# Optimization experiments

Hardware: AMD Instinct MI355X
Metric: run time of the kernel (lower is better)

The kernel has to match this reference:

```python
import jax, jax.numpy as jnp
import numpy as np
import math

M = 0.5
S = 64.0
TH = math.cos(math.pi - M)           # threshold cos(pi - m)
MM = math.sin(math.pi - M) * M       # sin(pi - m) * m
EPS = 1e-12

def _l2norm(x, axis=-1):
    return x / jnp.sqrt(jnp.sum(x * x, axis=axis, keepdims=True) + EPS)

def setup_inputs() -> dict:
    key = jax.random.key(0)
    k1, k2, k3 = jax.random.split(key, 3)
    B, D, C = 512, 512, 100000
    features = jax.random.normal(k1, (B, D), dtype=jnp.float32)
    weight = jax.random.normal(k2, (C, D), dtype=jnp.float32)
    labels = jax.random.randint(k3, (B,), 0, C, dtype=jnp.int32)
    return {"features": features, "labels": labels, "weight": weight}

def reference(features, labels, weight):
    # cos_theta: [B, C] = normalized features @ normalized weight^T
    cos_theta = jnp.einsum('bd,cd->bc', _l2norm(features), _l2norm(weight))
    cos_theta = jnp.clip(cos_theta, -1.0, 1.0)
    B = features.shape[0]
    rows = jnp.arange(B)
    # margin correction only affects the target column per row; gather it
    tgt_cos = cos_theta[rows, labels]                      # [B]
    theta_m = jnp.arccos(tgt_cos) + M
    cos_theta_m = jnp.cos(theta_m)
    tgt_adj = jnp.where(tgt_cos > TH, cos_theta_m, tgt_cos - MM)
    output = cos_theta.at[rows, labels].set(tgt_adj)
    return S * output
```

## Files before the change

### kernel.cpp

```cpp
#include <hip/hip_runtime.h>
#include <hip/hip_bf16.h>


typedef __attribute__((ext_vector_type(8))) short short8;
typedef __attribute__((ext_vector_type(8))) unsigned short u16x8;
typedef __attribute__((ext_vector_type(4))) float f32x4;

#define TH_CONST  (-0.8775825618903728f)
#define MM_CONST  (0.23971276930210156f)
#define M_MARGIN  0.5f
#define S_SCALE   64.0f

#define BM 128
#define BN 128
#define BK 32
#define KD 512

__device__ __forceinline__ unsigned short f2bf(float x) {
    unsigned int u = __float_as_uint(x);
    u += 0x7fffu + ((u >> 16) & 1u);
    return (unsigned short)(u >> 16);
}

__global__ __launch_bounds__(256, 2)
void arcface_kernel(const float* __restrict__ F,
                    const int*   __restrict__ labels,
                    const float* __restrict__ W,
                    float*       __restrict__ Out,
                    const int C)
{
    __shared__ unsigned short As[BM][BK];
    __shared__ unsigned short Bs[BN][BK];
    __shared__ float normF[BM];
    __shared__ float normW[BN];
    __shared__ int   Ls[BM];

    const int t = threadIdx.x;
    const int m_base = blockIdx.x * BM;
    const int n_base = blockIdx.y * BN;

    if (t < BM) Ls[t] = labels[m_base + t];

    const int r = t >> 1;
    const int h = t & 1;

    const int lane = t & 63;
    const int wave = t >> 6;
    const int wm = (wave >> 1) * 64;
    const int wn = (wave & 1) * 64;
    const int quad = lane >> 4;
    const int lcol = lane & 15;

    f32x4 acc[4][4];
    #pragma unroll
    for (int i = 0; i < 4; ++i)
        #pragma unroll
        for (int j = 0; j < 4; ++j)
            acc[i][j] = (f32x4){0.f, 0.f, 0.f, 0.f};

    const int cls = n_base + r;
    const bool cvalid = (cls < C);

    const float* Arow = F + (size_t)(m_base + r) * KD + h * 16;
    const float* Wrow = W + (size_t)(cvalid ? cls : 0) * KD + h * 16;

    float sF = 0.f, sW = 0.f;

    for (int kt = 0; kt < KD / BK; ++kt) {
        const float4* ap = (const float4*)(Arow + kt * BK);
        const float4* wp = (const float4*)(Wrow + kt * BK);
        float4 a0 = ap[0], a1 = ap[1], a2 = ap[2], a3 = ap[3];
        float4 w0, w1, w2, w3;
        if (cvalid) { w0 = wp[0]; w1 = wp[1]; w2 = wp[2]; w3 = wp[3]; }
        else {
            w0 = make_float4(0.f,0.f,0.f,0.f); w1 = w0; w2 = w0; w3 = w0;
        }

        sF += a0.x*a0.x + a0.y*a0.y + a0.z*a0.z + a0.w*a0.w
            + a1.x*a1.x + a1.y*a1.y + a1.z*a1.z + a1.w*a1.w
            + a2.x*a2.x + a2.y*a2.y + a2.z*a2.z + a2.w*a2.w
            + a3.x*a3.x + a3.y*a3.y + a3.z*a3.z + a3.w*a3.w;
        sW += w0.x*w0.x + w0.y*w0.y + w0.z*w0.z + w0.w*w0.w
            + w1.x*w1.x + w1.y*w1.y + w1.z*w1.z + w1.w*w1.w
            + w2.x*w2.x + w2.y*w2.y + w2.z*w2.z + w2.w*w2.w
            + w3.x*w3.x + w3.y*w3.y + w3.z*w3.z + w3.w*w3.w;

        u16x8 pa0, pa1, pb0, pb1;
        pa0[0]=f2bf(a0.x); pa0[1]=f2bf(a0.y); pa0[2]=f2bf(a0.z); pa0[3]=f2bf(a0.w);
        pa0[4]=f2bf(a1.x); pa0[5]=f2bf(a1.y); pa0[6]=f2bf(a1.z); pa0[7]=f2bf(a1.w);
        pa1[0]=f2bf(a2.x); pa1[1]=f2bf(a2.y); pa1[2]=f2bf(a2.z); pa1[3]=f2bf(a2.w);
        pa1[4]=f2bf(a3.x); pa1[5]=f2bf(a3.y); pa1[6]=f2bf(a3.z); pa1[7]=f2bf(a3.w);
        pb0[0]=f2bf(w0.x); pb0[1]=f2bf(w0.y); pb0[2]=f2bf(w0.z); pb0[3]=f2bf(w0.w);
        pb0[4]=f2bf(w1.x); pb0[5]=f2bf(w1.y); pb0[6]=f2bf(w1.z); pb0[7]=f2bf(w1.w);
        pb1[0]=f2bf(w2.x); pb1[1]=f2bf(w2.y); pb1[2]=f2bf(w2.z); pb1[3]=f2bf(w2.w);
        pb1[4]=f2bf(w3.x); pb1[5]=f2bf(w3.y); pb1[6]=f2bf(w3.z); pb1[7]=f2bf(w3.w);

        __syncthreads();
        *((u16x8*)&As[r][h*16])     = pa0;
        *((u16x8*)&As[r][h*16 + 8]) = pa1;
        *((u16x8*)&Bs[r][h*16])     = pb0;
        *((u16x8*)&Bs[r][h*16 + 8]) = pb1;
        __syncthreads();

        short8 af[4], bfr[4];
        #pragma unroll
        for (int i = 0; i < 4; ++i) {
            af[i]  = *(const short8*)&As[wm + i*16 + lcol][quad*8];
            bfr[i] = *(const short8*)&Bs[wn + i*16 + lcol][quad*8];
        }
        #pragma unroll
        for (int i = 0; i < 4; ++i)
            #pragma unroll
            for (int j = 0; j < 4; ++j)
                acc[i][j] = __builtin_amdgcn_mfma_f32_16x16x32_bf16(
                                af[i], bfr[j], acc[i][j], 0, 0, 0);
    }

    sF += __shfl_xor(sF, 1);
    sW += __shfl_xor(sW, 1);
    if (h == 0) {
        normF[r] = 1.0f / sqrtf(sF + 1e-12f);
        normW[r] = 1.0f / sqrtf(sW + 1e-12f);
    }
    __syncthreads();

    #pragma unroll
    for (int mi = 0; mi < 4; ++mi) {
        const int rl_base = wm + mi*16 + quad*4;
        #pragma unroll
        for (int rg = 0; rg < 4; ++rg) {
            const int rl = rl_base + rg;
            const float invf = normF[rl];
            const int lbl = Ls[rl];
            float* orow = Out + (size_t)(m_base + rl) * C;
            #pragma unroll
            for (int ni = 0; ni < 4; ++ni) {
                const int cl = wn + ni*16 + lcol;
                const int gcol = n_base + cl;
                if (gcol < C) {
                    float v = acc[mi][ni][rg] * invf * normW[cl];
                    v = fminf(1.0f, fmaxf(-1.0f, v));
                    if (gcol == lbl) {
                        v = (v > TH_CONST) ? cosf(acosf(v) + M_MARGIN)
                                           : (v - MM_CONST);
                    }
                    orow[gcol] = S_SCALE * v;
                }
            }
        }
    }
}

extern "C" void kernel_launch(void* const* d_in, const int* in_sizes, int n_in,
                              void* d_out, int out_size, void* d_ws, size_t ws_size,
                              hipStream_t stream) {
    const float* F      = (const float*)d_in[0];
    const int*   labels = (const int*)d_in[1];
    const float* W      = (const float*)d_in[2];
    float*       Out    = (float*)d_out;

    const int B = in_sizes[1];
    const int C = in_sizes[2] / KD;

    dim3 grid(B / BM, (C + BN - 1) / BN);
    arcface_kernel<<<grid, dim3(256), 0, stream>>>(F, labels, W, Out, C);
}
```

Measured before the change: 441.5 us.

## Precompute bf16 operands and norms, then GEMM with direct global-to-LDS loads

Adds a pre-pass kernel that converts W and F to bf16 once and computes the inverse L2 norms. A separate GEMM kernel then loads the bf16 tiles straight into LDS with global_load_lds and remaps workgroups across XCDs so blocks sharing the same W tile run on the same die. Previously every M-tile re-read the fp32 W rows and redid the conversion and norm work. The cost is an extra pass over W plus workspace writes, and a fallback to the old fused kernel when the workspace is too small.

```diff
diff --git a/kernel.cpp b/kernel.cpp
--- a/kernel.cpp
+++ b/kernel.cpp
@@ -1,5 +1,4 @@
 #include <hip/hip_runtime.h>
-#include <hip/hip_bf16.h>
 
 
 typedef __attribute__((ext_vector_type(8))) short short8;
@@ -10,10 +9,6 @@
 #define MM_CONST  (0.23971276930210156f)
 #define M_MARGIN  0.5f
 #define S_SCALE   64.0f
-
-#define BM 128
-#define BN 128
-#define BK 32
 #define KD 512
 
 __device__ __forceinline__ unsigned short f2bf(float x) {
@@ -22,12 +17,187 @@
     return (unsigned short)(u >> 16);
 }
 
+__global__ __launch_bounds__(256)
+void convert_norm_kernel(const float* __restrict__ W,
+                         const float* __restrict__ F,
+                         unsigned short* __restrict__ Wb,
+                         unsigned short* __restrict__ Fb,
+                         float* __restrict__ invW,
+                         float* __restrict__ invF,
+                         const int C, const int B)
+{
+    const int lane = threadIdx.x & 63;
+    int gw = blockIdx.x * 4 + (threadIdx.x >> 6);
+    const int stride = gridDim.x * 4;
+    const int total = C + B;
+
+    for (int row = gw; row < total; row += stride) {
+        const float* src;
+        unsigned short* dst;
+        float* inv;
+        if (row < C) {
+            src = W + (size_t)row * KD;
+            dst = Wb + (size_t)row * KD;
+            inv = invW + row;
+        } else {
+            const int r = row - C;
+            src = F + (size_t)r * KD;
+            dst = Fb + (size_t)r * KD;
+            inv = invF + r;
+        }
+        const float4* p = (const float4*)(src + lane * 8);
+        float4 v0 = p[0], v1 = p[1];
+
+        float ss = v0.x*v0.x + v0.y*v0.y + v0.z*v0.z + v0.w*v0.w
+                 + v1.x*v1.x + v1.y*v1.y + v1.z*v1.z + v1.w*v1.w;
+
+        u16x8 pk;
+        pk[0]=f2bf(v0.x); pk[1]=f2bf(v0.y); pk[2]=f2bf(v0.z); pk[3]=f2bf(v0.w);
+        pk[4]=f2bf(v1.x); pk[5]=f2bf(v1.y); pk[6]=f2bf(v1.z); pk[7]=f2bf(v1.w);
+        *(u16x8*)(dst + lane * 8) = pk;
+
+        ss += __shfl_xor(ss, 1);
+        ss += __shfl_xor(ss, 2);
+        ss += __shfl_xor(ss, 4);
+        ss += __shfl_xor(ss, 8);
+        ss += __shfl_xor(ss, 16);
+        ss += __shfl_xor(ss, 32);
+        if (lane == 0) *inv = 1.0f / sqrtf(ss + 1e-12f);
+    }
+}
+
+__device__ __forceinline__ void gload_lds_16(const void* g, void* l) {
+    __builtin_amdgcn_global_load_lds(
+        (const __attribute__((address_space(1))) unsigned int*)g,
+        (__attribute__((address_space(3))) unsigned int*)l,
+        16, 0, 0);
+}
+
 __global__ __launch_bounds__(256, 2)
-void arcface_kernel(const float* __restrict__ F,
-                    const int*   __restrict__ labels,
-                    const float* __restrict__ W,
-                    float*       __restrict__ Out,
-                    const int C)
+void arcface_gemm_kernel(const unsigned short* __restrict__ Fb,
+                         const unsigned short* __restrict__ Wb,
+                         const float* __restrict__ invF,
+                         const float* __restrict__ invW,
+                         const int*   __restrict__ labels,
+                         float*       __restrict__ Out,
+                         const int C, const int GM)
+{
+    __shared__ unsigned short As[128 * 32];
+    __shared__ unsigned short Bs[128 * 32];
+    __shared__ float nF[128];
+    __shared__ float nW[128];
+    __shared__ int   Ls[128];
+
+    const int nwg = gridDim.x;
+    const int bid = blockIdx.x;
+    const int q   = nwg >> 3, rr = nwg & 7;
+    const int xcd = bid & 7,  seq = bid >> 3;
+    const int wg  = (xcd < rr ? xcd * (q + 1) : rr * (q + 1) + (xcd - rr) * q) + seq;
+    const int mt  = wg % GM;
+    const int nt  = wg / GM;
+
+    const int m_base = mt * 128;
+    const int n_base = nt * 128;
+
+    const int t    = threadIdx.x;
+    const int wave = t >> 6;
+    const int lane = t & 63;
+    const int wm   = (wave >> 1) * 64;
+    const int wn   = (wave & 1) * 64;
+    const int quad = lane >> 4;
+    const int lcol = lane & 15;
+
+    if (t < 128) {
+        nF[t] = invF[m_base + t];
+        const int c = n_base + t;
+        nW[t] = (c < C) ? invW[c] : 0.f;
+        Ls[t] = labels[m_base + t];
+    }
+
+    const int off0 = t * 16;
+    const int ar0  = off0 >> 6;
+    const int cb0  = off0 & 63;
+    const int ar1  = ar0 + 64;
+
+    const char* gA0 = (const char*)Fb + (size_t)(m_base + ar0) * (KD * 2) + cb0;
+    const char* gA1 = (const char*)Fb + (size_t)(m_base + ar1) * (KD * 2) + cb0;
+    int b0 = n_base + ar0; if (b0 >= C) b0 = C - 1;
+    int b1 = n_base + ar1; if (b1 >= C) b1 = C - 1;
+    const char* gB0 = (const char*)Wb + (size_t)b0 * (KD * 2) + cb0;
+    const char* gB1 = (const char*)Wb + (size_t)b1 * (KD * 2) + cb0;
+
+    char* lA0 = (char*)As + wave * 1024;
+    char* lA1 = (char*)As + 4096 + wave * 1024;
+    char* lB0 = (char*)Bs + wave * 1024;
+    char* lB1 = (char*)Bs + 4096 + wave * 1024;
+
+    f32x4 acc[4][4];
+    #pragma unroll
+    for (int i = 0; i < 4; ++i)
+        #pragma unroll
+        for (int j = 0; j < 4; ++j)
+            acc[i][j] = (f32x4){0.f, 0.f, 0.f, 0.f};
+
+    #pragma unroll 1
+    for (int kt = 0; kt < KD / 32; ++kt) {
+        gload_lds_16(gA0 + kt * 64, lA0);
+        gload_lds_16(gA1 + kt * 64, lA1);
+        gload_lds_16(gB0 + kt * 64, lB0);
+        gload_lds_16(gB1 + kt * 64, lB1);
+        __syncthreads();
+
+        short8 af[4], bfr[4];
+        #pragma unroll
+        for (int i = 0; i < 4; ++i) {
+            af[i]  = *(const short8*)&As[(wm + i * 16 + lcol) * 32 + quad * 8];
+            bfr[i] = *(const short8*)&Bs[(wn + i * 16 + lcol) * 32 + quad * 8];
+        }
+        #pragma unroll
+        for (int i = 0; i < 4; ++i)
+            #pragma unroll
+            for (int j = 0; j < 4; ++j)
+                acc[i][j] = __builtin_amdgcn_mfma_f32_16x16x32_bf16(
+                                af[i], bfr[j], acc[i][j], 0, 0, 0);
+        __syncthreads();
+    }
+
+    #pragma unroll
+    for (int mi = 0; mi < 4; ++mi) {
+        const int rl_base = wm + mi * 16 + quad * 4;
+        #pragma unroll
+        for (int rg = 0; rg < 4; ++rg) {
+            const int rl = rl_base + rg;
+            const float invf = nF[rl];
+            const int lbl = Ls[rl];
+            float* orow = Out + (size_t)(m_base + rl) * C;
+            #pragma unroll
+            for (int ni = 0; ni < 4; ++ni) {
+                const int cl = wn + ni * 16 + lcol;
+                const int gcol = n_base + cl;
+                if (gcol < C) {
+                    float v = acc[mi][ni][rg] * invf * nW[cl];
+                    v = fminf(1.0f, fmaxf(-1.0f, v));
+                    if (gcol == lbl) {
+                        v = (v > TH_CONST) ? cosf(acosf(v) + M_MARGIN)
+                                           : (v - MM_CONST);
+                    }
+                    orow[gcol] = S_SCALE * v;
+                }
+            }
+        }
+    }
+}
+
+#define BM 128
+#define BN 128
+#define BK 32
+
+__global__ __launch_bounds__(256, 2)
+void arcface_fused_kernel(const float* __restrict__ F,
+                          const int*   __restrict__ labels,
+                          const float* __restrict__ W,
+                          float*       __restrict__ Out,
+                          const int C)
 {
     __shared__ unsigned short As[BM][BK];
     __shared__ unsigned short Bs[BN][BK];
@@ -72,9 +242,7 @@
         float4 a0 = ap[0], a1 = ap[1], a2 = ap[2], a3 = ap[3];
         float4 w0, w1, w2, w3;
         if (cvalid) { w0 = wp[0]; w1 = wp[1]; w2 = wp[2]; w3 = wp[3]; }
-        else {
-            w0 = make_float4(0.f,0.f,0.f,0.f); w1 = w0; w2 = w0; w3 = w0;
-        }
+        else { w0 = make_float4(0.f,0.f,0.f,0.f); w1 = w0; w2 = w0; w3 = w0; }
 
         sF += a0.x*a0.x + a0.y*a0.y + a0.z*a0.z + a0.w*a0.w
             + a1.x*a1.x + a1.y*a1.y + a1.z*a1.z + a1.w*a1.w
@@ -162,6 +330,31 @@
     const int B = in_sizes[1];
     const int C = in_sizes[2] / KD;
 
-    dim3 grid(B / BM, (C + BN - 1) / BN);
-    arcface_kernel<<<grid, dim3(256), 0, stream>>>(F, labels, W, Out, C);
-}
+    const size_t a = 255;
+    size_t offWb = 0;
+    size_t szWb  = (size_t)C * KD * sizeof(unsigned short);
+    size_t offFb = (offWb + szWb + a) & ~a;
+    size_t szFb  = (size_t)B * KD * sizeof(unsigned short);
+    size_t offIW = (offFb + szFb + a) & ~a;
+    size_t szIW  = (size_t)C * sizeof(float);
+    size_t offIF = (offIW + szIW + a) & ~a;
+    size_t szIF  = (size_t)B * sizeof(float);
+    size_t need  = offIF + szIF;
+
+    if (d_ws != nullptr && ws_size >= need && (B % 128) == 0) {
+        unsigned short* Wb   = (unsigned short*)((char*)d_ws + offWb);
+        unsigned short* Fb   = (unsigned short*)((char*)d_ws + offFb);
+        float*          invW = (float*)((char*)d_ws + offIW);
+        float*          invF = (float*)((char*)d_ws + offIF);
+
+        convert_norm_kernel<<<2048, 256, 0, stream>>>(W, F, Wb, Fb, invW, invF, C, B);
+
+        const int GM = B / 128;
+        const int NT = (C + 127) / 128;
+        arcface_gemm_kernel<<<GM * NT, 256, 0, stream>>>(Fb, Wb, invF, invW,
+                                                         labels, Out, C, GM);
+    } else {
+        dim3 grid(B / BM, (C + BN - 1) / BN);
+        arcface_fused_kernel<<<grid, dim3(256), 0, stream>>>(F, labels, W, Out, C);
+    }
+}
```

Result: slower. 462.9 us (+4.8%).

## Add double-buffered swizzled-LDS GEMM kernel with XCD-aware tile remapping

Applied to the files above, without the earlier changes.

Adds a new 512-thread kernel that uses BK=64 double-buffered LDS tiles, loading the next fp32 tile from global memory into registers while MFMAs run on the current buffer, with one barrier per k-step. LDS rows are XOR-swizzled to reduce bank conflicts, and the block index is remapped so that consecutive tiles sharing the same W columns land on the same XCD for L2 reuse. This cuts barrier count and exposed load latency, at the cost of more LDS per block and higher register pressure. The old kernel is kept as a fallback when B is not a multiple of 128.

```diff
diff --git a/kernel.cpp b/kernel.cpp
--- a/kernel.cpp
+++ b/kernel.cpp
@@ -3,18 +3,188 @@
 
 
 typedef __attribute__((ext_vector_type(8))) short short8;
-typedef __attribute__((ext_vector_type(8))) unsigned short u16x8;
 typedef __attribute__((ext_vector_type(4))) float f32x4;
 
 #define TH_CONST  (-0.8775825618903728f)
 #define MM_CONST  (0.23971276930210156f)
 #define M_MARGIN  0.5f
 #define S_SCALE   64.0f
-
-#define BM 128
-#define BN 128
-#define BK 32
 #define KD 512
+
+__device__ __forceinline__ unsigned short bfc(float x) {
+    union { __hip_bfloat16 h; unsigned short u; } cv;
+    cv.h = __float2bfloat16(x);
+    return cv.u;
+}
+
+__global__ __launch_bounds__(512, 4)
+void arcface_fused2(const float* __restrict__ F,
+                    const int*   __restrict__ labels,
+                    const float* __restrict__ W,
+                    float*       __restrict__ Out,
+                    const int C, const int GM)
+{
+    __shared__ __align__(16) unsigned short As[2][128 * 64];
+    __shared__ __align__(16) unsigned short Bs[2][128 * 64];
+    __shared__ float nF[128];
+    __shared__ float nW[128];
+    __shared__ int   Ls[128];
+
+    const int nwg = gridDim.x;
+    const int bid = blockIdx.x;
+    const int q   = nwg >> 3, rr = nwg & 7;
+    const int xcd = bid & 7,  seq = bid >> 3;
+    const int wg  = (xcd < rr ? xcd * (q + 1) : rr * (q + 1) + (xcd - rr) * q) + seq;
+    const int mt  = wg % GM;
+    const int nt  = wg / GM;
+    const int m_base = mt * 128;
+    const int n_base = nt * 128;
+
+    const int t    = threadIdx.x;
+    const int wave = t >> 6;
+    const int lane = t & 63;
+    const int wm   = (wave & 3) * 32;
+    const int wn   = (wave >> 2) * 64;
+    const int quad = lane >> 4;
+    const int lcol = lane & 15;
+
+    if (t < 128) Ls[t] = labels[m_base + t];
+
+    const int sg = t >> 4;
+    const int sc = t & 15;
+
+    unsigned int aOff[4], bOff[4];
+    int wof[4];
+    #pragma unroll
+    for (int i = 0; i < 4; ++i) {
+        const int rA = sg + 32 * i;
+        aOff[i] = (unsigned int)((m_base + rA) * KD + 4 * sc) * 4u;
+        int rB = n_base + rA;
+        if (rB >= C) rB = C - 1;
+        bOff[i] = (unsigned int)rB * (KD * 4u) + 16u * sc;
+        wof[i]  = rA * 64 + ((4 * sc) ^ ((rA & 7) << 3));
+    }
+
+    float sA[4] = {0.f, 0.f, 0.f, 0.f};
+    float sB[4] = {0.f, 0.f, 0.f, 0.f};
+    float4 va[4], vb[4];
+
+    const char* Fc = (const char*)F;
+    const char* Wc = (const char*)W;
+
+    f32x4 acc[2][4];
+    #pragma unroll
+    for (int i = 0; i < 2; ++i)
+        #pragma unroll
+        for (int j = 0; j < 4; ++j)
+            acc[i][j] = (f32x4){0.f, 0.f, 0.f, 0.f};
+
+    auto load_tile = [&](int kt) {
+        const unsigned int ko = (unsigned int)kt * 256u;
+        #pragma unroll
+        for (int i = 0; i < 4; ++i) {
+            va[i] = *(const float4*)(Fc + (aOff[i] + ko));
+            vb[i] = *(const float4*)(Wc + (bOff[i] + ko));
+        }
+    };
+
+    auto convert_write = [&](int nb) {
+        unsigned short* ab = As[nb];
+        unsigned short* bb = Bs[nb];
+        #pragma unroll
+        for (int i = 0; i < 4; ++i) {
+            float4 v = va[i];
+            sA[i] += v.x * v.x + v.y * v.y + v.z * v.z + v.w * v.w;
+            ushort4 p;
+            p.x = bfc(v.x); p.y = bfc(v.y); p.z = bfc(v.z); p.w = bfc(v.w);
+            *(ushort4*)&ab[wof[i]] = p;
+
+            float4 u = vb[i];
+            sB[i] += u.x * u.x + u.y * u.y + u.z * u.z + u.w * u.w;
+            ushort4 r;
+            r.x = bfc(u.x); r.y = bfc(u.y); r.z = bfc(u.z); r.w = bfc(u.w);
+            *(ushort4*)&bb[wof[i]] = r;
+        }
+    };
+
+    auto mfma_tile = [&](int cb) {
+        const unsigned short* ab = As[cb];
+        const unsigned short* bb = Bs[cb];
+        const int sw = (lcol & 7) << 3;
+        #pragma unroll
+        for (int h = 0; h < 2; ++h) {
+            const int co = (quad * 8 + 32 * h) ^ sw;
+            short8 af[2], bf_[4];
+            #pragma unroll
+            for (int i = 0; i < 2; ++i)
+                af[i] = *(const short8*)&ab[(wm + i * 16 + lcol) * 64 + co];
+            #pragma unroll
+            for (int j = 0; j < 4; ++j)
+                bf_[j] = *(const short8*)&bb[(wn + j * 16 + lcol) * 64 + co];
+            #pragma unroll
+            for (int i = 0; i < 2; ++i)
+                #pragma unroll
+                for (int j = 0; j < 4; ++j)
+                    acc[i][j] = __builtin_amdgcn_mfma_f32_16x16x32_bf16(
+                                    af[i], bf_[j], acc[i][j], 0, 0, 0);
+        }
+    };
+
+    load_tile(0);
+    convert_write(0);
+    __syncthreads();
+
+    #pragma unroll
+    for (int kt = 0; kt < KD / 64; ++kt) {
+        if (kt < KD / 64 - 1) load_tile(kt + 1);
+        mfma_tile(kt & 1);
+        if (kt < KD / 64 - 1) convert_write((kt + 1) & 1);
+        __syncthreads();
+    }
+
+    #pragma unroll
+    for (int i = 0; i < 4; ++i) {
+        float s = sA[i];
+        s += __shfl_xor(s, 1); s += __shfl_xor(s, 2);
+        s += __shfl_xor(s, 4); s += __shfl_xor(s, 8);
+        float w = sB[i];
+        w += __shfl_xor(w, 1); w += __shfl_xor(w, 2);
+        w += __shfl_xor(w, 4); w += __shfl_xor(w, 8);
+        if (sc == 0) {
+            nF[sg + 32 * i] = 1.0f / sqrtf(s + 1e-12f);
+            nW[sg + 32 * i] = 1.0f / sqrtf(w + 1e-12f);
+        }
+    }
+    __syncthreads();
+
+    #pragma unroll
+    for (int i = 0; i < 2; ++i) {
+        const int rl0 = wm + i * 16 + quad * 4;
+        #pragma unroll
+        for (int rg = 0; rg < 4; ++rg) {
+            const int rl = rl0 + rg;
+            const float invf = nF[rl];
+            const int lbl = Ls[rl];
+            float* orow = Out + (size_t)(m_base + rl) * C;
+            #pragma unroll
+            for (int j = 0; j < 4; ++j) {
+                const int cl = wn + j * 16 + lcol;
+                const int gcol = n_base + cl;
+                if (gcol < C) {
+                    float v = acc[i][j][rg] * invf * nW[cl];
+                    v = fminf(1.0f, fmaxf(-1.0f, v));
+                    if (gcol == lbl) {
+                        v = (v > TH_CONST) ? cosf(acosf(v) + M_MARGIN)
+                                           : (v - MM_CONST);
+                    }
+                    orow[gcol] = S_SCALE * v;
+                }
+            }
+        }
+    }
+}
+
+typedef __attribute__((ext_vector_type(8))) unsigned short u16x8;
 
 __device__ __forceinline__ unsigned short f2bf(float x) {
     unsigned int u = __float_as_uint(x);
@@ -22,24 +192,28 @@
     return (unsigned short)(u >> 16);
 }
 
+#define BM 128
+#define BN 128
+#define BK 32
+
 __global__ __launch_bounds__(256, 2)
-void arcface_kernel(const float* __restrict__ F,
-                    const int*   __restrict__ labels,
-                    const float* __restrict__ W,
-                    float*       __restrict__ Out,
-                    const int C)
+void arcface_fused_kernel(const float* __restrict__ F,
+                          const int*   __restrict__ labels,
+                          const float* __restrict__ W,
+                          float*       __restrict__ Out,
+                          const int C)
 {
-    __shared__ unsigned short As[BM][BK];
-    __shared__ unsigned short Bs[BN][BK];
+    __shared__ unsigned short Asf[BM][BK];
+    __shared__ unsigned short Bsf[BN][BK];
     __shared__ float normF[BM];
     __shared__ float normW[BN];
-    __shared__ int   Ls[BM];
+    __shared__ int   Lsf[BM];
 
     const int t = threadIdx.x;
     const int m_base = blockIdx.x * BM;
     const int n_base = blockIdx.y * BN;
 
-    if (t < BM) Ls[t] = labels[m_base + t];
+    if (t < BM) Lsf[t] = labels[m_base + t];
 
     const int r = t >> 1;
     const int h = t & 1;
@@ -72,9 +246,7 @@
         float4 a0 = ap[0], a1 = ap[1], a2 = ap[2], a3 = ap[3];
         float4 w0, w1, w2, w3;
         if (cvalid) { w0 = wp[0]; w1 = wp[1]; w2 = wp[2]; w3 = wp[3]; }
-        else {
-            w0 = make_float4(0.f,0.f,0.f,0.f); w1 = w0; w2 = w0; w3 = w0;
-        }
+        else { w0 = make_float4(0.f,0.f,0.f,0.f); w1 = w0; w2 = w0; w3 = w0; }
 
         sF += a0.x*a0.x + a0.y*a0.y + a0.z*a0.z + a0.w*a0.w
             + a1.x*a1.x + a1.y*a1.y + a1.z*a1.z + a1.w*a1.w
@@ -96,17 +268,17 @@
         pb1[4]=f2bf(w3.x); pb1[5]=f2bf(w3.y); pb1[6]=f2bf(w3.z); pb1[7]=f2bf(w3.w);
 
         __syncthreads();
-        *((u16x8*)&As[r][h*16])     = pa0;
-        *((u16x8*)&As[r][h*16 + 8]) = pa1;
-        *((u16x8*)&Bs[r][h*16])     = pb0;
-        *((u16x8*)&Bs[r][h*16 + 8]) = pb1;
+        *((u16x8*)&Asf[r][h*16])     = pa0;
+        *((u16x8*)&Asf[r][h*16 + 8]) = pa1;
+        *((u16x8*)&Bsf[r][h*16])     = pb0;
+        *((u16x8*)&Bsf[r][h*16 + 8]) = pb1;
         __syncthreads();
 
         short8 af[4], bfr[4];
         #pragma unroll
         for (int i = 0; i < 4; ++i) {
-            af[i]  = *(const short8*)&As[wm + i*16 + lcol][quad*8];
-            bfr[i] = *(const short8*)&Bs[wn + i*16 + lcol][quad*8];
+            af[i]  = *(const short8*)&Asf[wm + i*16 + lcol][quad*8];
+            bfr[i] = *(const short8*)&Bsf[wn + i*16 + lcol][quad*8];
         }
         #pragma unroll
         for (int i = 0; i < 4; ++i)
@@ -131,7 +303,7 @@
         for (int rg = 0; rg < 4; ++rg) {
             const int rl = rl_base + rg;
             const float invf = normF[rl];
-            const int lbl = Ls[rl];
+            const int lbl = Lsf[rl];
             float* orow = Out + (size_t)(m_base + rl) * C;
             #pragma unroll
             for (int ni = 0; ni < 4; ++ni) {
@@ -162,6 +334,12 @@
     const int B = in_sizes[1];
     const int C = in_sizes[2] / KD;
 
-    dim3 grid(B / BM, (C + BN - 1) / BN);
-    arcface_kernel<<<grid, dim3(256), 0, stream>>>(F, labels, W, Out, C);
-}
+    if ((B % 128) == 0) {
+        const int GM = B / 128;
+        const int NT = (C + 127) / 128;
+        arcface_fused2<<<GM * NT, dim3(512), 0, stream>>>(F, labels, W, Out, C, GM);
+    } else {
+        dim3 grid((B + BM - 1) / BM, (C + BN - 1) / BN);
+        arcface_fused_kernel<<<grid, dim3(256), 0, stream>>>(F, labels, W, Out, C);
+    }
+}
```

New measurement: 770.0 us. +74.4%, slower.
